# Kernel optimization log

Hardware: AMD Instinct MI355X
Metric: run time of the kernel (lower is better)

Reference implementation:

```python
import jax, jax.numpy as jnp
import numpy as np

DIM_MODEL = 2048
DQK = 64
DV = 64
NUM_HEADS = 32
NUM_GROUPS = 8
H_PER_G = NUM_HEADS // NUM_GROUPS
ROPE_THETA = 10000.0
RMS_EPS = 1e-6


def _rope(x):
    # x: [b, g, h, s, d]; rotate-half RoPE over last dim, positions along s.
    d = x.shape[-1]
    s = x.shape[-2]
    inv_freq = 1.0 / (ROPE_THETA ** (jnp.arange(0, d, 2, dtype=jnp.float32) / d))  # [d/2]
    ang = jnp.arange(s, dtype=jnp.float32)[:, None] * inv_freq[None, :]  # [s, d/2]
    cos, sin = jnp.cos(ang), jnp.sin(ang)
    x1, x2 = x[..., : d // 2], x[..., d // 2 :]
    return jnp.concatenate([x1 * cos - x2 * sin, x2 * cos + x1 * sin], axis=-1)


def setup_inputs() -> dict:
    key = jax.random.key(0)
    k1, k2, k3 = jax.random.split(key, 3)
    b, s = 2, 2048
    concat = NUM_HEADS * DQK + NUM_GROUPS * (DQK + DV)  # 3072
    x = jax.random.normal(k1, (b, s, DIM_MODEL), dtype=jnp.float32)
    w_in = jax.random.normal(k2, (concat, DIM_MODEL), dtype=jnp.float32) * (DIM_MODEL ** -0.5)
    w_out = jax.random.normal(k3, (DIM_MODEL, NUM_HEADS * DV), dtype=jnp.float32) * ((NUM_HEADS * DV) ** -0.5)
    rms_w = jnp.ones((DIM_MODEL,), dtype=jnp.float32)
    return {"x": x, "w_in": w_in, "w_out": w_out, "rms_w": rms_w}


def reference(x, w_in, w_out, rms_w):
    b, s, _ = x.shape
    # RMSNorm
    y = x * jax.lax.rsqrt(jnp.mean(x * x, axis=-1, keepdims=True) + RMS_EPS) * rms_w
    # In-projection (Linear, no bias): y @ w_in.T
    y = jnp.einsum('bsm,cm->bsc', y, w_in)
    cq = NUM_HEADS * DQK
    ck = NUM_GROUPS * DQK
    q, k, v = y[..., :cq], y[..., cq:cq + ck], y[..., cq + ck:]
    # q: b s (g h d) -> b g h s d ; k,v: b s (g d) -> b g 1 s d
    q = q.reshape(b, s, NUM_GROUPS, H_PER_G, DQK).transpose(0, 2, 3, 1, 4)
    k = k.reshape(b, s, NUM_GROUPS, DQK).transpose(0, 2, 1, 3)[:, :, None]
    v = v.reshape(b, s, NUM_GROUPS, DV).transpose(0, 2, 1, 3)[:, :, None]
    q = _rope(q)
    k = _rope(k)
    # scores with GQA broadcast over h
    qk = jnp.einsum('bghsd,bgxpd->bghsp', q, k) * (DQK ** -0.5)
    causal = jnp.tril(jnp.ones((s, s), dtype=bool))
    qk = jnp.where(causal, qk, -jnp.inf)
    attn = jax.nn.softmax(qk, axis=-1)
    o = jnp.einsum('bghsp,bgxpd->bghsd', attn, v)  # [b,g,h,s,d]
    o = o.transpose(0, 3, 1, 2, 4).reshape(b, s, NUM_HEADS * DV)
    y = jnp.einsum('bsc,mc->bsm', o, w_out)
    return x + y
```

## Files before the change

### kernel.cpp

```cpp
#include <hip/hip_runtime.h>
#include <hip/hip_bf16.h>

#define TOKENS   4096
#define SEQ      2048
#define DMODEL   2048
#define CONCAT   3072
#define NHEADS   32
#define NGROUPS  8
#define HPERG    4
#define CQ       2048
#define CK       512

typedef __attribute__((ext_vector_type(8))) short bf16x8;
typedef __attribute__((ext_vector_type(4))) float f32x4;

__device__ __forceinline__ ushort f2bf(float f) {
    __hip_bfloat16 h = __float2bfloat16(f);
    return __builtin_bit_cast(ushort, h);
}

__device__ __forceinline__ uint cvt_pk_bf16(float lo, float hi) {
    uint r;
    asm("v_cvt_pk_bf16_f32 %0, %1, %2" : "=v"(r) : "v"(lo), "v"(hi));
    return r;
}

#define GLOBAL_TO_LDS16(g, l)                                                  \
    __builtin_amdgcn_global_load_lds(                                          \
        (const __attribute__((address_space(1))) void*)(g),                    \
        (__attribute__((address_space(3))) void*)(l), 16, 0, 0)

#define PREP_ROPE 256
#define PREP_RMS  (PREP_ROPE + TOKENS)
#define N4_WIN  (CONCAT * DMODEL / 4)
#define N4_WOUT (DMODEL * DMODEL / 4)
#define PREP_TOTAL (PREP_RMS + (N4_WIN + N4_WOUT + 255) / 256)

__global__ void prep_kernel(const float* __restrict__ x,
                            const float* __restrict__ rms_w,
                            const float* __restrict__ w_in,
                            const float* __restrict__ w_out,
                            ushort* __restrict__ y_bf,
                            ushort* __restrict__ w_in_bf,
                            ushort* __restrict__ w_out_bf,
                            float2* __restrict__ tab) {
    int blk = blockIdx.x, tid = threadIdx.x;
    if (blk < PREP_ROPE) {
        int i = blk * 256 + tid;
        int s = i >> 5, j = i & 31;
        const float LOG2_THETA = 13.287712379549449f;
        float inv = exp2f(-((float)j / 32.0f) * LOG2_THETA);
        float ang = (float)s * inv;
        tab[i] = make_float2(cosf(ang), sinf(ang));
    } else if (blk < PREP_RMS) {
        int t = blk - PREP_ROPE;
        const float4* xr = (const float4*)(x + (size_t)t * DMODEL);
        float4 v[2];
        float ss = 0.f;
#pragma unroll
        for (int i = 0; i < 2; i++) {
            v[i] = xr[tid + i * 256];
            ss += v[i].x * v[i].x + v[i].y * v[i].y + v[i].z * v[i].z + v[i].w * v[i].w;
        }
#pragma unroll
        for (int off = 32; off >= 1; off >>= 1) ss += __shfl_xor(ss, off);
        __shared__ float red[4];
        int wid = tid >> 6;
        if ((tid & 63) == 0) red[wid] = ss;
        __syncthreads();
        float total = red[0] + red[1] + red[2] + red[3];
        float scale = rsqrtf(total * (1.0f / DMODEL) + 1e-6f);
        const float4* wr = (const float4*)rms_w;
        ushort4* yr = (ushort4*)(y_bf + (size_t)t * DMODEL);
#pragma unroll
        for (int i = 0; i < 2; i++) {
            int c = tid + i * 256;
            float4 wv = wr[c];
            ushort4 o;
            o.x = f2bf(v[i].x * scale * wv.x);
            o.y = f2bf(v[i].y * scale * wv.y);
            o.z = f2bf(v[i].z * scale * wv.z);
            o.w = f2bf(v[i].w * scale * wv.w);
            yr[c] = o;
        }
    } else {
        int i = (blk - PREP_RMS) * 256 + tid;
        const float* src;
        ushort* dst;
        int j;
        if (i < N4_WIN) { src = w_in; dst = w_in_bf; j = i; }
        else if (i < N4_WIN + N4_WOUT) { src = w_out; dst = w_out_bf; j = i - N4_WIN; }
        else return;
        float4 v = ((const float4*)src)[j];
        ushort4 o;
        o.x = f2bf(v.x); o.y = f2bf(v.y); o.z = f2bf(v.z); o.w = f2bf(v.w);
        ((ushort4*)dst)[j] = o;
    }
}

#define LGKM(nn) asm volatile("s_waitcnt lgkmcnt(" #nn ")" ::: "memory")
#define VMC(nn)  asm volatile("s_waitcnt vmcnt(" #nn ")" ::: "memory")
#define SBAR()   __builtin_amdgcn_s_barrier()
#define SCHED0() __builtin_amdgcn_sched_barrier(0)
#define PRIO(p)  __builtin_amdgcn_s_setprio(p)

#define RD_A(mh)                                                              \
    _Pragma("unroll") for (int mi = 0; mi < 4; mi++)                          \
    _Pragma("unroll") for (int ks = 0; ks < 2; ks++)                          \
        af[mi][ks] = *(const bf16x8*)(Ab +                                    \
            ((arow0 + (mh) * 64 + mi * 16) * 8 +                              \
             ((ks * 4 + quad) ^ an)) * 8);

#define RD_B(nh)                                                              \
    _Pragma("unroll") for (int ni = 0; ni < NFRAG; ni++)                      \
    _Pragma("unroll") for (int ks = 0; ks < 2; ks++)                          \
        bfr[nh][ni][ks] = *(const bf16x8*)(Bb +                               \
            ((brow0 + (nh) * (16 * NFRAG) + ni * 16) * 8 +                    \
             ((ks * 4 + quad) ^ an)) * 8);

#define MMQ(mh, nh)                                                           \
    _Pragma("unroll") for (int mi = 0; mi < 4; mi++)                          \
    _Pragma("unroll") for (int ni = 0; ni < NFRAG; ni++)                      \
    _Pragma("unroll") for (int ks = 0; ks < 2; ks++)                          \
        acc[(mh) * 4 + mi][(nh) * NFRAG + ni] =                               \
            __builtin_amdgcn_mfma_f32_16x16x32_bf16(af[mi][ks],               \
                bfr[nh][ni][ks], acc[(mh) * 4 + mi][(nh) * NFRAG + ni],       \
                0, 0, 0);

#define ISSUE_HALF(H_)                                                        \
    {                                                                         \
        int H = (H_);                                                         \
        if (H < 4 * NT) {                                                     \
            int t2 = H >> 2, j2 = H & 3;                                      \
            int k0 = t2 << 6;                                                 \
            if (j2 == 0 || j2 == 3) {                                         \
                int half = (j2 == 3);                                         \
                ushort* lb = (ushort*)&As[t2 & 1][0];                         \
                _Pragma("unroll") for (int c = 0; c < 2; c++) {               \
                    int s = w * 2 + c;                                        \
                    int row = (s >> 3) * 128 + half * 64 + (s & 7) * 8;       \
                    const ushort* g = Aptr +                                  \
                        (size_t)(bm + row + l8) * K + k0 + kb8;               \
                    GLOBAL_TO_LDS16(g, lb + row * 64);                        \
                }                                                             \
            } else {                                                          \
                int half = (j2 == 2);                                         \
                ushort* lb = (ushort*)&Bs[t2 & 1][0];                         \
                if constexpr (NFRAG == 2) {                                   \
                    _Pragma("unroll") for (int c = 0; c < 2; c++) {           \
                        int s = w * 2 + c;                                    \
                        int row = (s >> 2) * 64 + half * 32 + (s & 3) * 8;    \
                        const ushort* g = Bptr +                              \
                            (size_t)(bn + row + l8) * K + k0 + kb8;           \
                        GLOBAL_TO_LDS16(g, lb + row * 64);                    \
                    }                                                         \
                } else {                                                      \
                    int row = (w >> 1) * 32 + half * 16 + (w & 1) * 8;        \
                    const ushort* g = Bptr +                                  \
                        (size_t)(bn + row + l8) * K + k0 + kb8;               \
                    GLOBAL_TO_LDS16(g, lb + row * 64);                        \
                }                                                             \
            }                                                                 \
        }                                                                     \
    }

#define VMC_STEADY()                                                          \
    { if constexpr (NFRAG == 2) { VMC(6); } else { VMC(4); } }

#define TILE(t_, BUF)                                                         \
    {                                                                         \
        const ushort* Ab = &As[BUF][0];                                       \
        const ushort* Bb = &Bs[BUF][0];                                       \
                                                \
        RD_A(0); RD_B(0);                                                     \
        ISSUE_HALF(4 * (t_) + 7);                                             \
        LGKM(8);                                                              \
        SBAR(); LGKM(0); SCHED0();                                            \
        PRIO(1); MMQ(0, 0); PRIO(0);                                          \
        SBAR();                                                               \
                                                   \
        RD_B(1);                                                              \
        ISSUE_HALF(4 * (t_) + 8);                                             \
        SBAR(); LGKM(0); SCHED0();                                            \
        PRIO(1); MMQ(0, 1); PRIO(0);                                          \
        SBAR();                                                               \
                                                   \
        RD_A(1);                                                              \
        ISSUE_HALF(4 * (t_) + 9);                                             \
        SBAR(); LGKM(0); SCHED0();                                            \
        PRIO(1); MMQ(1, 0); PRIO(0);                                          \
        SBAR();                                                               \
                           \
        ISSUE_HALF(4 * (t_) + 10);                                            \
        SBAR(); SCHED0();                                                     \
        PRIO(1); MMQ(1, 1); PRIO(0);                                          \
        if ((t_) + 2 < NT)        { VMC_STEADY(); }                           \
        else if ((t_) + 2 == NT)  { VMC(0); }                                 \
        SBAR();                                                               \
    }

template <int EPI, int NFRAG>
__global__ __launch_bounds__(512, 2) void gemm_nt_8ph(
        const ushort* __restrict__ Aptr, const ushort* __restrict__ Bptr,
        const float* __restrict__ X, float* __restrict__ OUT,
        ushort* __restrict__ Qb_, ushort* __restrict__ Kb_,
        ushort* __restrict__ Vb_, const float2* __restrict__ Tab,
        int M, int N, int K) {
    __shared__ __align__(16) ushort As[2][256 * 64];
    __shared__ __align__(16) ushort Bs[2][NFRAG * 128 * 64];

    int nwg = (int)(gridDim.x * gridDim.y);
    int lin = (int)(blockIdx.y * gridDim.x + blockIdx.x);
    int swz = lin;
    if ((nwg & 7) == 0) swz = (lin & 7) * (nwg >> 3) + (lin >> 3);
    const int bm = (swz / (int)gridDim.x) * 256;
    const int bn = (swz % (int)gridDim.x) * (128 * NFRAG);

    const int w = threadIdx.x >> 6, lane = threadIdx.x & 63;
    const int n = lane & 15, quad = lane >> 4;
    const int wm = w >> 2, wn = w & 3;
    const int an = n & 7;
    const int l8 = lane >> 3;
    const int kb8 = ((lane & 7) ^ l8) * 8;
    const int arow0 = wm * 128 + n;
    const int brow0 = wn * (32 * NFRAG) + n;
    const int NT = K >> 6;

    f32x4 acc[8][2 * NFRAG] = {};
    bf16x8 af[4][2], bfr[2][NFRAG][2];

    ISSUE_HALF(0); ISSUE_HALF(1); ISSUE_HALF(2); ISSUE_HALF(3);
    ISSUE_HALF(4); ISSUE_HALF(5); ISSUE_HALF(6);
    VMC_STEADY();
    SBAR();

    for (int tt = 0; tt < NT; tt += 2) {
        TILE(tt, 0);
        TILE(tt + 1, 1);
    }

    if constexpr (EPI == 2) {
        const int bq = bm >> 11;
        const int s0 = bm & 2047;
        int col0 = bn + wn * 64;
        int slb = wm * 128 + quad * 4;
        if (col0 < CQ + CK) {
            bool isQ = col0 < CQ;
            ushort* base;
            if (isQ) {
                int head = col0 >> 6;
                base = Qb_ + ((size_t)((bq * 8 + (head >> 2)) * 4 + (head & 3))
                              * SEQ) * 64;
            } else {
                int kh = (col0 - CQ) >> 6;
                base = Kb_ + ((size_t)(bq * 8 + kh) * SEQ) * 64;
            }
            const float QS = 0.18033688011112042f;
#pragma unroll
            for (int mi = 0; mi < 8; mi++)
#pragma unroll
                for (int r = 0; r < 4; r++) {
                    int s = s0 + slb + mi * 16 + r;
                    float2 t0 = Tab[(size_t)s * 32 + n];
                    float2 t1 = Tab[(size_t)s * 32 + n + 16];
                    float o1a = acc[mi][0][r] * t0.x - acc[mi][2][r] * t0.y;
                    float o2a = acc[mi][2][r] * t0.x + acc[mi][0][r] * t0.y;
                    float o1b = acc[mi][1][r] * t1.x - acc[mi][3][r] * t1.y;
                    float o2b = acc[mi][3][r] * t1.x + acc[mi][1][r] * t1.y;
                    if (isQ) { o1a *= QS; o2a *= QS; o1b *= QS; o2b *= QS; }
                    uint* drow = (uint*)(base + (size_t)s * 64);
                    drow[n]      = cvt_pk_bf16(o1a, o2a);
                    drow[16 + n] = cvt_pk_bf16(o1b, o2b);
                }
        } else {
            int vh = (col0 - CQ - CK) >> 6;
            ushort* vb = Vb_ + (size_t)(bq * 8 + vh) * 64 * SEQ;
#pragma unroll
            for (int mi = 0; mi < 8; mi++)
#pragma unroll
                for (int ni = 0; ni < 2 * NFRAG; ni++) {
                    int d = ni * 16 + n;
                    int s = s0 + slb + mi * 16;
                    uint* dst = (uint*)(vb + (size_t)d * SEQ + s);
                    dst[0] = cvt_pk_bf16(acc[mi][ni][0], acc[mi][ni][1]);
                    dst[1] = cvt_pk_bf16(acc[mi][ni][2], acc[mi][ni][3]);
                }
        }
    } else {
#pragma unroll
        for (int mi = 0; mi < 8; mi++)
#pragma unroll
            for (int ni = 0; ni < 2 * NFRAG; ni++) {
                int c0 = bm + wm * 128 + mi * 16 + quad * 4;
                int t  = bn + wn * (32 * NFRAG) + ni * 16 + n;
                const float4 xv = *(const float4*)(X + (size_t)t * DMODEL + c0);
                float4 ov;
                ov.x = xv.x + acc[mi][ni][0];
                ov.y = xv.y + acc[mi][ni][1];
                ov.z = xv.z + acc[mi][ni][2];
                ov.w = xv.w + acc[mi][ni][3];
                *(float4*)(OUT + (size_t)t * DMODEL + c0) = ov;
            }
    }
}

#define AISSUE(kt_, buf_)                                                     \
    {                                                                         \
        const ushort* Kg_ = Kg0 + (kt_) * 64 * 64;                            \
        const ushort* Vg_ = Vg0 + (kt_) * 64;                                 \
        GLOBAL_TO_LDS16(Kg_ + (w * 8 + l3) * 64 + lx * 8,                     \
                        &Kl[buf_][(size_t)threadIdx.x * 8]);                  \
        GLOBAL_TO_LDS16(Vg_ + (size_t)(w * 8 + l3) * SEQ + lx * 8,            \
                        &Vl[buf_][(size_t)threadIdx.x * 8]);                  \
    }

__global__ __launch_bounds__(512) void attn_mfma_kernel(
        const ushort* __restrict__ Qb, const ushort* __restrict__ Kb,
        const ushort* __restrict__ Vb, ushort* __restrict__ o_bf) {
    __shared__ __align__(16) ushort Kl[2][512 * 8];
    __shared__ __align__(16) ushort Vl[2][512 * 8];
    __shared__ __align__(16) uint   Pl[8][544];

    int blk = blockIdx.x;
    int qt  = 15 - (blk >> 6);
    int bgh = blk & 63;
    int h = bgh & 3, g = (bgh >> 2) & 7, b = bgh >> 5;
    int w = threadIdx.x >> 6, lane = threadIdx.x & 63;
    int n = lane & 15, quad = lane >> 4;
    const int an = n & 7;
    int Q0 = qt * 128;
    int qw = Q0 + w * 16;

    const int l3 = lane >> 3;
    const int lx = (lane & 7) ^ l3;

    const ushort* Qh  = Qb + (size_t)((b * 8 + g) * 4 + h) * (SEQ * 64);
    const ushort* Kg0 = Kb + (size_t)(b * 8 + g) * (SEQ * 64);
    const ushort* Vg0 = Vb + (size_t)(b * 8 + g) * (64 * SEQ);

    bf16x8 aq[2];
#pragma unroll
    for (int ks = 0; ks < 2; ks++)
        aq[ks] = *(const bf16x8*)(
            Qh + (size_t)(qw + n) * 64 + ks * 32 + quad * 8);

    f32x4 od[4] = {};
    f32x4 od4 = {};

    short onev = (n == 0) ? (short)0x3F80 : (short)0;
    bf16x8 bones = {onev, onev, onev, onev, onev, onev, onev, onev};

    uint* Pw = Pl[w];
    int nkt = qt * 2 + 2;

    AISSUE(0, 0);
    AISSUE(1, 1);

    for (int kt = 0; kt < nkt; kt++) {
        int buf = kt & 1;
        if (kt + 1 < nkt) { VMC(2); } else { VMC(0); }
        SBAR(); SCHED0();

        bool act = (kt * 64 <= qw + 15);
        if (act) {
            const ushort* Kb_ = Kl[buf];
            const ushort* Vb_ = Vl[buf];

#pragma unroll
            for (int t16k = 0; t16k < 4; t16k++) {
                int krow = (t16k * 16 + n) * 8;
                bf16x8 kf0 = *(const bf16x8*)(Kb_ + (krow + (quad ^ an)) * 8);
                bf16x8 kf1 = *(const bf16x8*)(Kb_ + (krow + ((quad + 4) ^ an)) * 8);
                int key0 = kt * 64 + t16k * 16 + quad * 4;
                f32x4 c = {};
                PRIO(1);
                c = __builtin_amdgcn_mfma_f32_16x16x32_bf16(kf0, aq[0], c, 0, 0, 0);
                c = __builtin_amdgcn_mfma_f32_16x16x32_bf16(kf1, aq[1], c, 0, 0, 0);
                PRIO(0);
                int qrow = qw + n;
                float p[4];
                if (kt * 64 + 63 > qw) {
#pragma unroll
                    for (int r = 0; r < 4; r++)
                        p[r] = (key0 + r <= qrow) ? __builtin_amdgcn_exp2f(c[r]) : 0.f;
                } else {
#pragma unroll
                    for (int r = 0; r < 4; r++)
                        p[r] = __builtin_amdgcn_exp2f(c[r]);
                }
                uint d0 = cvt_pk_bf16(p[0], p[1]);
                uint d1 = cvt_pk_bf16(p[2], p[3]);
                int base = ((t16k * 2 + (quad >> 1)) * 17 + n) * 4
                           + (quad & 1) * 2;
                Pw[base]     = d0;
                Pw[base + 1] = d1;
            }

#pragma unroll
            for (int kb2 = 0; kb2 < 2; kb2++) {
                int kb = kb2 * 4 + quad;
                bf16x8 bv[4];
#pragma unroll
                for (int dt = 0; dt < 4; dt++)
                    bv[dt] = *(const bf16x8*)(Vb_ +
                        (((dt * 16 + n) * 8 + (kb ^ an)) * 8));
                bf16x8 ap = *(const bf16x8*)(
                    (const ushort*)Pw + ((kb2 * 4 + quad) * 17 + n) * 8);
                PRIO(1);
#pragma unroll
                for (int dt = 0; dt < 4; dt++)
                    od[dt] = __builtin_amdgcn_mfma_f32_16x16x32_bf16(
                        ap, bv[dt], od[dt], 0, 0, 0);
                od4 = __builtin_amdgcn_mfma_f32_16x16x32_bf16(
                    ap, bones, od4, 0, 0, 0);
                PRIO(0);
            }
        }

        SCHED0(); SBAR();
        if (kt + 2 < nkt) AISSUE(kt + 2, buf);
    }

    float linv[4];
#pragma unroll
    for (int r = 0; r < 4; r++) {
        float lv = __shfl(od4[r], lane & 48);
        linv[r] = __builtin_amdgcn_rcpf(lv);
    }
#pragma unroll
    for (int dt = 0; dt < 4; dt++)
#pragma unroll
        for (int r = 0; r < 4; r++) {
            int q = qw + quad * 4 + r;
            int col = (g * 4 + h) * 64 + dt * 16 + n;
            o_bf[(size_t)(b * SEQ + q) * DMODEL + col] =
                f2bf(od[dt][r] * linv[r]);
        }
}

extern "C" void kernel_launch(void* const* d_in, const int* in_sizes, int n_in,
                              void* d_out, int out_size, void* d_ws, size_t ws_size,
                              hipStream_t stream) {
    const float* x     = (const float*)d_in[0];
    const float* w_in  = (const float*)d_in[1];
    const float* w_out = (const float*)d_in[2];
    const float* rms_w = (const float*)d_in[3];
    float* out = (float*)d_out;

    const size_t MB = 1024 * 1024;
    char* ws = (char*)d_ws;
    ushort* Qb       = (ushort*)ws;
    ushort* Kb       = (ushort*)(ws + 16 * MB);
    ushort* Vb       = (ushort*)(ws + 20 * MB);
    ushort* o_bf     = (ushort*)(ws + 24 * MB);
    float2* rope_tab = (float2*)(ws + 24 * MB);
    ushort* w_out_bf = (ushort*)(ws + 40 * MB);
    ushort* y_bf     = (ushort*)(ws + 48 * MB);
    ushort* w_in_bf  = (ushort*)(ws + 64 * MB);

    prep_kernel<<<PREP_TOTAL, 256, 0, stream>>>(
        x, rms_w, w_in, w_out, y_bf, w_in_bf, w_out_bf, rope_tab);

    gemm_nt_8ph<2, 2><<<dim3(CONCAT / 256, TOKENS / 256), 512, 0, stream>>>(
        y_bf, w_in_bf, nullptr, nullptr, Qb, Kb, Vb, rope_tab,
        TOKENS, CONCAT, DMODEL);

    attn_mfma_kernel<<<1024, 512, 0, stream>>>(Qb, Kb, Vb, o_bf);

    gemm_nt_8ph<3, 1><<<dim3(TOKENS / 128, DMODEL / 256), 512, 0, stream>>>(
        w_out_bf, o_bf, x, out, nullptr, nullptr, nullptr, nullptr,
        DMODEL, TOKENS, DMODEL);
}
```

Baseline: 277.7 us.

## Replace out-projection GEMM with dedicated 128x128-tile kernel and specialize in-projection

The templated GEMM is split in two. The in-projection becomes a non-templated kernel fixed at 256x256 tiles with the RoPE/QKV epilogue. The out-projection gets a new simpler kernel with 128x128 tiles, a 2-stage double buffer, and 4 blocks per CU, giving 512 workgroups instead of 256. The aim is better occupancy and tail balance on the out-projection, at the cost of less reuse per tile and a simpler pipeline with full barriers each k-step.

```diff
diff --git a/kernel.cpp b/kernel.cpp
--- a/kernel.cpp
+++ b/kernel.cpp
@@ -112,19 +112,19 @@
              ((ks * 4 + quad) ^ an)) * 8);
 
 #define RD_B(nh)                                                              \
-    _Pragma("unroll") for (int ni = 0; ni < NFRAG; ni++)                      \
+    _Pragma("unroll") for (int ni = 0; ni < 2; ni++)                          \
     _Pragma("unroll") for (int ks = 0; ks < 2; ks++)                          \
         bfr[nh][ni][ks] = *(const bf16x8*)(Bb +                               \
-            ((brow0 + (nh) * (16 * NFRAG) + ni * 16) * 8 +                    \
+            ((brow0 + (nh) * 32 + ni * 16) * 8 +                              \
              ((ks * 4 + quad) ^ an)) * 8);
 
 #define MMQ(mh, nh)                                                           \
     _Pragma("unroll") for (int mi = 0; mi < 4; mi++)                          \
-    _Pragma("unroll") for (int ni = 0; ni < NFRAG; ni++)                      \
+    _Pragma("unroll") for (int ni = 0; ni < 2; ni++)                          \
     _Pragma("unroll") for (int ks = 0; ks < 2; ks++)                          \
-        acc[(mh) * 4 + mi][(nh) * NFRAG + ni] =                               \
+        acc[(mh) * 4 + mi][(nh) * 2 + ni] =                                   \
             __builtin_amdgcn_mfma_f32_16x16x32_bf16(af[mi][ks],               \
-                bfr[nh][ni][ks], acc[(mh) * 4 + mi][(nh) * NFRAG + ni],       \
+                bfr[nh][ni][ks], acc[(mh) * 4 + mi][(nh) * 2 + ni],           \
                 0, 0, 0);
 
 #define ISSUE_HALF(H_)                                                        \
@@ -146,16 +146,9 @@
             } else {                                                          \
                 int half = (j2 == 2);                                         \
                 ushort* lb = (ushort*)&Bs[t2 & 1][0];                         \
-                if constexpr (NFRAG == 2) {                                   \
-                    _Pragma("unroll") for (int c = 0; c < 2; c++) {           \
-                        int s = w * 2 + c;                                    \
-                        int row = (s >> 2) * 64 + half * 32 + (s & 3) * 8;    \
-                        const ushort* g = Bptr +                              \
-                            (size_t)(bn + row + l8) * K + k0 + kb8;           \
-                        GLOBAL_TO_LDS16(g, lb + row * 64);                    \
-                    }                                                         \
-                } else {                                                      \
-                    int row = (w >> 1) * 32 + half * 16 + (w & 1) * 8;        \
+                _Pragma("unroll") for (int c = 0; c < 2; c++) {               \
+                    int s = w * 2 + c;                                        \
+                    int row = (s >> 2) * 64 + half * 32 + (s & 3) * 8;        \
                     const ushort* g = Bptr +                                  \
                         (size_t)(bn + row + l8) * K + k0 + kb8;               \
                     GLOBAL_TO_LDS16(g, lb + row * 64);                        \
@@ -163,9 +156,6 @@
             }                                                                 \
         }                                                                     \
     }
-
-#define VMC_STEADY()                                                          \
-    { if constexpr (NFRAG == 2) { VMC(6); } else { VMC(4); } }
 
 #define TILE(t_, BUF)                                                         \
     {                                                                         \
@@ -194,27 +184,24 @@
         ISSUE_HALF(4 * (t_) + 10);                                            \
         SBAR(); SCHED0();                                                     \
         PRIO(1); MMQ(1, 1); PRIO(0);                                          \
-        if ((t_) + 2 < NT)        { VMC_STEADY(); }                           \
+        if ((t_) + 2 < NT)        { VMC(6); }                                 \
         else if ((t_) + 2 == NT)  { VMC(0); }                                 \
         SBAR();                                                               \
     }
 
-template <int EPI, int NFRAG>
-__global__ __launch_bounds__(512, 2) void gemm_nt_8ph(
+__global__ __launch_bounds__(512, 2) void gemm_in_8ph(
         const ushort* __restrict__ Aptr, const ushort* __restrict__ Bptr,
-        const float* __restrict__ X, float* __restrict__ OUT,
         ushort* __restrict__ Qb_, ushort* __restrict__ Kb_,
         ushort* __restrict__ Vb_, const float2* __restrict__ Tab,
         int M, int N, int K) {
     __shared__ __align__(16) ushort As[2][256 * 64];
-    __shared__ __align__(16) ushort Bs[2][NFRAG * 128 * 64];
+    __shared__ __align__(16) ushort Bs[2][256 * 64];
 
     int nwg = (int)(gridDim.x * gridDim.y);
     int lin = (int)(blockIdx.y * gridDim.x + blockIdx.x);
-    int swz = lin;
-    if ((nwg & 7) == 0) swz = (lin & 7) * (nwg >> 3) + (lin >> 3);
+    int swz = (lin & 7) * (nwg >> 3) + (lin >> 3);
     const int bm = (swz / (int)gridDim.x) * 256;
-    const int bn = (swz % (int)gridDim.x) * (128 * NFRAG);
+    const int bn = (swz % (int)gridDim.x) * 256;
 
     const int w = threadIdx.x >> 6, lane = threadIdx.x & 63;
     const int n = lane & 15, quad = lane >> 4;
@@ -223,15 +210,15 @@
     const int l8 = lane >> 3;
     const int kb8 = ((lane & 7) ^ l8) * 8;
     const int arow0 = wm * 128 + n;
-    const int brow0 = wn * (32 * NFRAG) + n;
+    const int brow0 = wn * 64 + n;
     const int NT = K >> 6;
 
-    f32x4 acc[8][2 * NFRAG] = {};
-    bf16x8 af[4][2], bfr[2][NFRAG][2];
+    f32x4 acc[8][4] = {};
+    bf16x8 af[4][2], bfr[2][2][2];
 
     ISSUE_HALF(0); ISSUE_HALF(1); ISSUE_HALF(2); ISSUE_HALF(3);
     ISSUE_HALF(4); ISSUE_HALF(5); ISSUE_HALF(6);
-    VMC_STEADY();
+    VMC(6);
     SBAR();
 
     for (int tt = 0; tt < NT; tt += 2) {
@@ -239,69 +226,142 @@
         TILE(tt + 1, 1);
     }
 
-    if constexpr (EPI == 2) {
-        const int bq = bm >> 11;
-        const int s0 = bm & 2047;
-        int col0 = bn + wn * 64;
-        int slb = wm * 128 + quad * 4;
-        if (col0 < CQ + CK) {
-            bool isQ = col0 < CQ;
-            ushort* base;
-            if (isQ) {
-                int head = col0 >> 6;
-                base = Qb_ + ((size_t)((bq * 8 + (head >> 2)) * 4 + (head & 3))
-                              * SEQ) * 64;
-            } else {
-                int kh = (col0 - CQ) >> 6;
-                base = Kb_ + ((size_t)(bq * 8 + kh) * SEQ) * 64;
+    const int bq = bm >> 11;
+    const int s0 = bm & 2047;
+    int col0 = bn + wn * 64;
+    int slb = wm * 128 + quad * 4;
+    if (col0 < CQ + CK) {
+        bool isQ = col0 < CQ;
+        ushort* base;
+        if (isQ) {
+            int head = col0 >> 6;
+            base = Qb_ + ((size_t)((bq * 8 + (head >> 2)) * 4 + (head & 3))
+                          * SEQ) * 64;
+        } else {
+            int kh = (col0 - CQ) >> 6;
+            base = Kb_ + ((size_t)(bq * 8 + kh) * SEQ) * 64;
+        }
+        const float QS = 0.18033688011112042f;
+#pragma unroll
+        for (int mi = 0; mi < 8; mi++)
+#pragma unroll
+            for (int r = 0; r < 4; r++) {
+                int s = s0 + slb + mi * 16 + r;
+                float2 t0 = Tab[(size_t)s * 32 + n];
+                float2 t1 = Tab[(size_t)s * 32 + n + 16];
+                float o1a = acc[mi][0][r] * t0.x - acc[mi][2][r] * t0.y;
+                float o2a = acc[mi][2][r] * t0.x + acc[mi][0][r] * t0.y;
+                float o1b = acc[mi][1][r] * t1.x - acc[mi][3][r] * t1.y;
+                float o2b = acc[mi][3][r] * t1.x + acc[mi][1][r] * t1.y;
+                if (isQ) { o1a *= QS; o2a *= QS; o1b *= QS; o2b *= QS; }
+                uint* drow = (uint*)(base + (size_t)s * 64);
+                drow[n]      = cvt_pk_bf16(o1a, o2a);
+                drow[16 + n] = cvt_pk_bf16(o1b, o2b);
             }
-            const float QS = 0.18033688011112042f;
-#pragma unroll
-            for (int mi = 0; mi < 8; mi++)
-#pragma unroll
-                for (int r = 0; r < 4; r++) {
-                    int s = s0 + slb + mi * 16 + r;
-                    float2 t0 = Tab[(size_t)s * 32 + n];
-                    float2 t1 = Tab[(size_t)s * 32 + n + 16];
-                    float o1a = acc[mi][0][r] * t0.x - acc[mi][2][r] * t0.y;
-                    float o2a = acc[mi][2][r] * t0.x + acc[mi][0][r] * t0.y;
-                    float o1b = acc[mi][1][r] * t1.x - acc[mi][3][r] * t1.y;
-                    float o2b = acc[mi][3][r] * t1.x + acc[mi][1][r] * t1.y;
-                    if (isQ) { o1a *= QS; o2a *= QS; o1b *= QS; o2b *= QS; }
-                    uint* drow = (uint*)(base + (size_t)s * 64);
-                    drow[n]      = cvt_pk_bf16(o1a, o2a);
-                    drow[16 + n] = cvt_pk_bf16(o1b, o2b);
-                }
-        } else {
-            int vh = (col0 - CQ - CK) >> 6;
-            ushort* vb = Vb_ + (size_t)(bq * 8 + vh) * 64 * SEQ;
-#pragma unroll
-            for (int mi = 0; mi < 8; mi++)
-#pragma unroll
-                for (int ni = 0; ni < 2 * NFRAG; ni++) {
-                    int d = ni * 16 + n;
-                    int s = s0 + slb + mi * 16;
-                    uint* dst = (uint*)(vb + (size_t)d * SEQ + s);
-                    dst[0] = cvt_pk_bf16(acc[mi][ni][0], acc[mi][ni][1]);
-                    dst[1] = cvt_pk_bf16(acc[mi][ni][2], acc[mi][ni][3]);
-                }
+    } else {
+        int vh = (col0 - CQ - CK) >> 6;
+        ushort* vb = Vb_ + (size_t)(bq * 8 + vh) * 64 * SEQ;
+#pragma unroll
+        for (int mi = 0; mi < 8; mi++)
+#pragma unroll
+            for (int ni = 0; ni < 4; ni++) {
+                int d = ni * 16 + n;
+                int s = s0 + slb + mi * 16;
+                uint* dst = (uint*)(vb + (size_t)d * SEQ + s);
+                dst[0] = cvt_pk_bf16(acc[mi][ni][0], acc[mi][ni][1]);
+                dst[1] = cvt_pk_bf16(acc[mi][ni][2], acc[mi][ni][3]);
+            }
+    }
+}
+
+#define OSTAGE(t_, b_)                                                        \
+    {                                                                         \
+        int k0 = (t_) << 6;                                                   \
+        _Pragma("unroll") for (int c = 0; c < 2; c++) {                       \
+            int row = c * 64 + w * 8 + l3;                                    \
+            GLOBAL_TO_LDS16(Aptr + (size_t)(bm + row) * DMODEL + k0 + kx8,    \
+                            &As[b_][(c * 64 + w * 8) * 64]);                  \
+            GLOBAL_TO_LDS16(Bptr + (size_t)(bn + row) * DMODEL + k0 + kx8,    \
+                            &Bs[b_][(c * 64 + w * 8) * 64]);                  \
+        }                                                                     \
+    }
+
+__global__ __launch_bounds__(512, 4) void gemm_out_128(
+        const ushort* __restrict__ Aptr,
+        const ushort* __restrict__ Bptr,
+        const float* __restrict__ X, float* __restrict__ OUT) {
+    __shared__ __align__(16) ushort As[2][128 * 64];
+    __shared__ __align__(16) ushort Bs[2][128 * 64];
+    const int NT = DMODEL >> 6;
+
+    int nwg = (int)(gridDim.x * gridDim.y);
+    int lin = (int)(blockIdx.y * gridDim.x + blockIdx.x);
+    int swz = (lin & 7) * (nwg >> 3) + (lin >> 3);
+    const int bm = (swz / (int)gridDim.x) * 128;
+    const int bn = (swz % (int)gridDim.x) * 128;
+
+    const int w = threadIdx.x >> 6, lane = threadIdx.x & 63;
+    const int n = lane & 15, quad = lane >> 4;
+    const int wm = w >> 2, wn = w & 3;
+    const int an = n & 7;
+    const int l3 = lane >> 3;
+    const int kx8 = ((lane & 7) ^ l3) * 8;
+
+    f32x4 acc[4][2] = {};
+    bf16x8 af[4][2], bfr[2][2];
+
+    OSTAGE(0, 0);
+    OSTAGE(1, 1);
+    VMC(4);
+    SBAR();
+
+    for (int t = 0; t < NT; t++) {
+        int b = t & 1;
+#pragma unroll
+        for (int mi = 0; mi < 4; mi++)
+#pragma unroll
+            for (int ks = 0; ks < 2; ks++)
+                af[mi][ks] = *(const bf16x8*)(&As[b][0] +
+                    ((wm * 64 + mi * 16 + n) * 8 + ((ks * 4 + quad) ^ an)) * 8);
+#pragma unroll
+        for (int ni = 0; ni < 2; ni++)
+#pragma unroll
+            for (int ks = 0; ks < 2; ks++)
+                bfr[ni][ks] = *(const bf16x8*)(&Bs[b][0] +
+                    ((wn * 32 + ni * 16 + n) * 8 + ((ks * 4 + quad) ^ an)) * 8);
+        LGKM(0);
+        SBAR();
+        if (t + 2 < NT) OSTAGE(t + 2, b);
+        SCHED0();
+        PRIO(1);
+#pragma unroll
+        for (int mi = 0; mi < 4; mi++)
+#pragma unroll
+            for (int ni = 0; ni < 2; ni++)
+#pragma unroll
+                for (int ks = 0; ks < 2; ks++)
+                    acc[mi][ni] = __builtin_amdgcn_mfma_f32_16x16x32_bf16(
+                        af[mi][ks], bfr[ni][ks], acc[mi][ni], 0, 0, 0);
+        PRIO(0);
+        if (t + 2 < NT)      { VMC(4); }
+        else if (t + 1 < NT) { VMC(0); }
+        SBAR();
+    }
+
+#pragma unroll
+    for (int mi = 0; mi < 4; mi++)
+#pragma unroll
+        for (int ni = 0; ni < 2; ni++) {
+            int c0 = bm + wm * 64 + mi * 16 + quad * 4;
+            int t  = bn + wn * 32 + ni * 16 + n;
+            const float4 xv = *(const float4*)(X + (size_t)t * DMODEL + c0);
+            float4 ov;
+            ov.x = xv.x + acc[mi][ni][0];
+            ov.y = xv.y + acc[mi][ni][1];
+            ov.z = xv.z + acc[mi][ni][2];
+            ov.w = xv.w + acc[mi][ni][3];
+            *(float4*)(OUT + (size_t)t * DMODEL + c0) = ov;
         }
-    } else {
-#pragma unroll
-        for (int mi = 0; mi < 8; mi++)
-#pragma unroll
-            for (int ni = 0; ni < 2 * NFRAG; ni++) {
-                int c0 = bm + wm * 128 + mi * 16 + quad * 4;
-                int t  = bn + wn * (32 * NFRAG) + ni * 16 + n;
-                const float4 xv = *(const float4*)(X + (size_t)t * DMODEL + c0);
-                float4 ov;
-                ov.x = xv.x + acc[mi][ni][0];
-                ov.y = xv.y + acc[mi][ni][1];
-                ov.z = xv.z + acc[mi][ni][2];
-                ov.w = xv.w + acc[mi][ni][3];
-                *(float4*)(OUT + (size_t)t * DMODEL + c0) = ov;
-            }
-    }
 }
 
 #define AISSUE(kt_, buf_)                                                     \
@@ -461,13 +521,11 @@
     prep_kernel<<<PREP_TOTAL, 256, 0, stream>>>(
         x, rms_w, w_in, w_out, y_bf, w_in_bf, w_out_bf, rope_tab);
 
-    gemm_nt_8ph<2, 2><<<dim3(CONCAT / 256, TOKENS / 256), 512, 0, stream>>>(
-        y_bf, w_in_bf, nullptr, nullptr, Qb, Kb, Vb, rope_tab,
-        TOKENS, CONCAT, DMODEL);
+    gemm_in_8ph<<<dim3(CONCAT / 256, TOKENS / 256), 512, 0, stream>>>(
+        y_bf, w_in_bf, Qb, Kb, Vb, rope_tab, TOKENS, CONCAT, DMODEL);
 
     attn_mfma_kernel<<<1024, 512, 0, stream>>>(Qb, Kb, Vb, o_bf);
 
-    gemm_nt_8ph<3, 1><<<dim3(TOKENS / 128, DMODEL / 256), 512, 0, stream>>>(
-        w_out_bf, o_bf, x, out, nullptr, nullptr, nullptr, nullptr,
-        DMODEL, TOKENS, DMODEL);
-}
+    gemm_out_128<<<dim3(TOKENS / 128, DMODEL / 128), 512, 0, stream>>>(
+        w_out_bf, o_bf, x, out);
+}
```

Result: faster. 262.4 us (-5.5%).
